# Kernel optimization log

Measured on AMD Instinct MI355X. Metric: run time of the kernel, lower is better.

## Reference

```python
import jax, jax.numpy as jnp
import numpy as np

H = 4  # heads_n (sequential refinement heads)


def _layer_norm(x, g, b, eps=1e-5):
    mu = jnp.mean(x, axis=-1, keepdims=True)
    var = jnp.mean((x - mu) ** 2, axis=-1, keepdims=True)
    return (x - mu) * jax.lax.rsqrt(var + eps) * g + b


def _pose_enc(S, F):
    # Faithful translation of PoseEncoding._make_pe_buffer
    pos = jnp.arange(S, dtype=jnp.float32)[:, None]            # (S,1)
    div = (1.0 / (1000.0 ** (2.0 * jnp.arange(F, dtype=jnp.float32) / F)))[None, :]  # (1,F)
    pe = jnp.zeros((S, F), jnp.float32)
    pe = pe.at[0::2, :].set(jnp.sin(pos[0::2] * div))
    pe = pe.at[1::2, :].set(jnp.cos(pos[1::2] * div))
    return pe  # (S,F)


def setup_inputs() -> dict:
    key = jax.random.key(0)
    ks = jax.random.split(key, 6)
    B, S, C = 4, 2048, 1024
    std = 0.02
    return {
        "x": jax.random.normal(ks[0], (B, S, C), jnp.float32),
        "fc_in_w": jax.random.normal(ks[1], (C, C), jnp.float32) * std,
        "fc_in_b": jnp.zeros((C,), jnp.float32),
        "ln_g": jnp.ones((C,), jnp.float32),
        "ln_b": jnp.zeros((C,), jnp.float32),
        "qkv_w": jax.random.normal(ks[2], (H, 3 * C, C), jnp.float32) * std,
        "qkv_b": jnp.zeros((H, 3 * C), jnp.float32),
        "proj_w": jax.random.normal(ks[3], (H, C, C), jnp.float32) * std,
        "proj_b": jnp.zeros((H, C), jnp.float32),
        "fc_out_w": jax.random.normal(ks[4], (C, C), jnp.float32) * std,
        "fc_out_b": jnp.zeros((C,), jnp.float32),
    }


def reference(x, fc_in_w, fc_in_b, ln_g, ln_b, qkv_w, qkv_b, proj_w, proj_b, fc_out_w, fc_out_b):
    B, S, C = x.shape
    gelu = lambda t: jax.nn.gelu(t, approximate=False)  # nn.GELU default = exact erf
    h = x @ fc_in_w.T + fc_in_b                         # fc_in
    h = _layer_norm(h, ln_g, ln_b)
    pred = None
    for i in range(qkv_w.shape[0]):                     # sequential heads loop (eval mode: dropout = identity)
        qkv = gelu(h @ qkv_w[i].T + qkv_b[i])           # (B,S,3C)
        qkv = qkv.reshape(B, S, 3, C)
        q, k, v = qkv[:, :, 0], qkv[:, :, 1], qkv[:, :, 2]
        scores = jnp.einsum('bsc,btc->bst', q, k) * (1.0 / C)  # (B,S,S), mask is None
        att = jnp.einsum('bst,btc->bsc', scores, v)     # matmul BEFORE softmax (non-standard order)
        att = jax.nn.softmax(att, axis=-1)
        h = gelu(att @ proj_w[i].T + proj_b[i])
        if pred is None:
            pred = h
        else:
            h = h + pred                                 # residual with first head's output
    out = h @ fc_out_w.T + fc_out_b
    return out + _pose_enc(S, out.shape[-1])[None]      # PoseEncoding add
```

## Files before the change

### kernel.cpp

```cpp
#include <hip/hip_runtime.h>
#include <math.h>

typedef unsigned short u16;
typedef __bf16 bf16x8 __attribute__((ext_vector_type(8)));
typedef float f32x4  __attribute__((ext_vector_type(4)));
typedef float f32x16 __attribute__((ext_vector_type(16)));
typedef u16   u16x4  __attribute__((ext_vector_type(4)));
typedef u16   u16x8  __attribute__((ext_vector_type(8)));

#define GPTR(p) ((__attribute__((address_space(1))) void*)(p))
#define LPTR(p) ((__attribute__((address_space(3))) void*)(p))

__device__ __forceinline__ float bf2f(u16 h) { return __uint_as_float(((unsigned)h) << 16); }
__device__ __forceinline__ u16 f2bf(float f) {
    unsigned u = __float_as_uint(f);
    return (u16)((u + 0x7fffu + ((u >> 16) & 1u)) >> 16);
}
__device__ __forceinline__ float gelu_f(float x) {
    float u = 0.7978845608f * x * (1.0f + 0.044715f * x * x);
    float e = __expf(2.0f * u);
    float t = 1.0f - 2.0f / (e + 1.0f);
    return 0.5f * x * (1.0f + t);
}

template<int MODE, int BG>
__global__ __launch_bounds__(256, 4)
void gemm_bt(const u16* __restrict__ A, int lda, long sA,
             const u16* __restrict__ B, int ldb, long sB,
             void* __restrict__ Cout, int ldc, long sC,
             const float* __restrict__ bias,
             const u16* __restrict__ addend,
             int K, float scale)
{
    __shared__ u16 lds[BG ? 8192 : 16384];
    u16* lA = lds;
    u16* lB = lds + 8192;
    const int t    = threadIdx.x;
    const int lane = t & 63;
    const int wid  = t >> 6;
    const int wm   = (wid & 1) * 64;
    const int wn   = (wid >> 1) * 64;
    const int m32  = lane & 31;
    const int h    = lane >> 5;
    const int bz   = blockIdx.z;

    const long rowA0 = (long)blockIdx.y * 128;
    const long colB0 = (long)blockIdx.x * 128;
    const u16* Ab = A + (long)bz * sA + rowA0 * lda;

    const int rt  = t >> 3;
    const int kcg = ((t & 7) ^ (rt & 7)) * 8;
    const u16* gA[4];
    #pragma unroll
    for (int j = 0; j < 4; j++) gA[j] = Ab + (long)(j * 32 + rt) * lda + kcg;
    u16* dA = lA + t * 8;

    const u16* gB[4]; u16* dB = lB + t * 8;
    const u16* gb0 = nullptr; const u16* gb1 = nullptr;
    if constexpr (BG) {
        const int nt0 = (int)((colB0 + wn) >> 5);
        gb0 = B + (long)nt0 * (K >> 4) * 512 + lane * 8;
        gb1 = gb0 + (long)(K >> 4) * 512;
    } else {
        const u16* Bb = B + (long)bz * sB + colB0 * ldb;
        #pragma unroll
        for (int j = 0; j < 4; j++) gB[j] = Bb + (long)(j * 32 + rt) * ldb + kcg;
    }

    f32x16 acc[2][2];
    #pragma unroll
    for (int i = 0; i < 2; i++)
        #pragma unroll
        for (int j = 0; j < 2; j++)
            #pragma unroll
            for (int r = 0; r < 16; r++) acc[i][j][r] = 0.f;

    const int sg = m32 & 7;
    const u16* fA[4]; const u16* fB[4];
    #pragma unroll
    for (int kh = 0; kh < 4; kh++) {
        fA[kh] = lA + (wm + m32) * 64 + 8 * ((kh * 2 + h) ^ sg);
        if constexpr (!BG) fB[kh] = lB + (wn + m32) * 64 + 8 * ((kh * 2 + h) ^ sg);
    }

    for (int k0 = 0; k0 < K; k0 += 64) {
        #pragma unroll
        for (int j = 0; j < 4; j++)
            __builtin_amdgcn_global_load_lds(GPTR(gA[j] + k0), LPTR(dA + j * 2048), 16, 0, 0);
        bf16x8 bg[2][4];
        if constexpr (BG) {
            #pragma unroll
            for (int kh = 0; kh < 4; kh++) {
                bg[0][kh] = *(const bf16x8*)(gb0 + (long)k0 * 32 + kh * 512);
                bg[1][kh] = *(const bf16x8*)(gb1 + (long)k0 * 32 + kh * 512);
            }
        } else {
            #pragma unroll
            for (int j = 0; j < 4; j++)
                __builtin_amdgcn_global_load_lds(GPTR(gB[j] + k0), LPTR(dB + j * 2048), 16, 0, 0);
        }
        __syncthreads();
        #pragma unroll
        for (int kh = 0; kh < 4; kh++) {
            bf16x8 a0 = *(const bf16x8*)(fA[kh]);
            bf16x8 a1 = *(const bf16x8*)(fA[kh] + 2048);
            bf16x8 b0, b1;
            if constexpr (BG) { b0 = bg[0][kh]; b1 = bg[1][kh]; }
            else {
                b0 = *(const bf16x8*)(fB[kh]);
                b1 = *(const bf16x8*)(fB[kh] + 2048);
            }
            acc[0][0] = __builtin_amdgcn_mfma_f32_32x32x16_bf16(a0, b0, acc[0][0], 0, 0, 0);
            acc[0][1] = __builtin_amdgcn_mfma_f32_32x32x16_bf16(a0, b1, acc[0][1], 0, 0, 0);
            acc[1][0] = __builtin_amdgcn_mfma_f32_32x32x16_bf16(a1, b0, acc[1][0], 0, 0, 0);
            acc[1][1] = __builtin_amdgcn_mfma_f32_32x32x16_bf16(a1, b1, acc[1][1], 0, 0, 0);
        }
        __syncthreads();
    }

    float* Cf = (float*)Cout + (long)bz * sC;
    u16*   Cu = (u16*)Cout + (long)bz * sC;
    float* sw_ = (float*)lds + wid * 1024;
    const long rb = rowA0 + wm;
    const long cb = colB0 + wn;
    const int prow = lane >> 3;
    const int c4   = (lane & 7) * 4;
    #pragma unroll
    for (int mi = 0; mi < 2; mi++) {
        #pragma unroll
        for (int ni = 0; ni < 2; ni++) {
            #pragma unroll
            for (int r = 0; r < 16; r++)
                sw_[((r & 3) + 8 * (r >> 2) + 4 * h) * 32 + m32] = acc[mi][ni][r];
            #pragma unroll
            for (int p = 0; p < 4; p++) {
                const int  row  = p * 8 + prow;
                const long grow = rb + mi * 32 + row;
                const long gcol = cb + ni * 32 + c4;
                f32x4 v = *(const f32x4*)&sw_[row * 32 + c4];
                float4 bvv = {0.f, 0.f, 0.f, 0.f};
                if constexpr (MODE >= 2) bvv = *(const float4*)&bias[gcol];
                if constexpr (MODE == 1) {
                    #pragma unroll
                    for (int e = 0; e < 4; e++) v[e] *= scale;
                }
                v[0] += bvv.x; v[1] += bvv.y; v[2] += bvv.z; v[3] += bvv.w;
                if constexpr (MODE == 3 || MODE == 4) {
                    #pragma unroll
                    for (int e = 0; e < 4; e++) v[e] = gelu_f(v[e]);
                }
                if constexpr (MODE == 4) {
                    u16x4 ad = *(const u16x4*)&addend[grow * (long)ldc + gcol];
                    #pragma unroll
                    for (int e = 0; e < 4; e++) v[e] += bf2f(ad[e]);
                }
                if constexpr (MODE == 5) {
                    *(f32x4*)&Cf[grow * (long)ldc + gcol] = v;
                } else {
                    u16x4 o = { f2bf(v[0]), f2bf(v[1]), f2bf(v[2]), f2bf(v[3]) };
                    *(u16x4*)&Cu[grow * (long)ldc + gcol] = o;
                }
            }
        }
    }
}

__global__ __launch_bounds__(256)
void cvt_x(const float* __restrict__ in, u16* __restrict__ out, long n)
{
    long i = ((long)blockIdx.x * 256 + threadIdx.x) * 4;
    if (i < n) {
        float4 v = *(const float4*)(in + i);
        u16x4 o = { f2bf(v.x), f2bf(v.y), f2bf(v.z), f2bf(v.w) };
        *(u16x4*)(out + i) = o;
    }
}

__global__ __launch_bounds__(256)
void cvt_wg(const float* __restrict__ qkvw, u16* __restrict__ dqkv,
            const float* __restrict__ projw, u16* __restrict__ dproj,
            const float* __restrict__ fciw, u16* __restrict__ dfci,
            const float* __restrict__ fcow, u16* __restrict__ dfco)
{
    __shared__ u16 sl[2048];
    const int nt = blockIdx.y;
    const int ks = blockIdx.x;
    const int t  = threadIdx.x;
    const float* src; u16* dst; int nl;
    if      (nt < 384) { src = qkvw;  dst = dqkv;  nl = nt; }
    else if (nt < 512) { src = projw; dst = dproj; nl = nt - 384; }
    else if (nt < 544) { src = fciw;  dst = dfci;  nl = nt - 512; }
    else               { src = fcow;  dst = dfco;  nl = nt - 544; }
    const int n32 = t >> 3;
    const int kq  = t & 7;
    const float* s = src + ((long)nl * 32 + n32) * 1024 + ks * 64 + kq * 8;
    float4 v0 = *(const float4*)s;
    float4 v1 = *(const float4*)(s + 4);
    u16x8 o = { f2bf(v0.x), f2bf(v0.y), f2bf(v0.z), f2bf(v0.w),
                f2bf(v1.x), f2bf(v1.y), f2bf(v1.z), f2bf(v1.w) };
    const int slot = (kq >> 1) * 64 + (kq & 1) * 32 + n32;
    *(u16x8*)&sl[slot * 8] = o;
    __syncthreads();
    u16* d = dst + (long)nl * 32768 + ks * 2048 + t * 8;
    *(u16x8*)d = *(const u16x8*)&sl[t * 8];
}

__global__ __launch_bounds__(256)
void ln_kernel(const u16* __restrict__ in, u16* __restrict__ out,
               const float* __restrict__ g, const float* __restrict__ b)
{
    const int row = blockIdx.x;
    const int t = threadIdx.x;
    const u16* r = in + (long)row * 1024;
    float x[4];
    float s = 0.f, s2 = 0.f;
    #pragma unroll
    for (int j = 0; j < 4; j++) { x[j] = bf2f(r[t + 256 * j]); s += x[j]; s2 += x[j] * x[j]; }
    __shared__ float sm[8];
    const int lane = t & 63, wid = t >> 6;
    #pragma unroll
    for (int o = 32; o > 0; o >>= 1) { s += __shfl_down(s, o, 64); s2 += __shfl_down(s2, o, 64); }
    if (lane == 0) { sm[wid] = s; sm[4 + wid] = s2; }
    __syncthreads();
    s  = sm[0] + sm[1] + sm[2] + sm[3];
    s2 = sm[4] + sm[5] + sm[6] + sm[7];
    const float mean = s * (1.f / 1024.f);
    const float var  = s2 * (1.f / 1024.f) - mean * mean;
    const float rstd = rsqrtf(var + 1e-5f);
    u16* o = out + (long)row * 1024;
    #pragma unroll
    for (int j = 0; j < 4; j++) {
        int c = t + 256 * j;
        o[c] = f2bf((x[j] - mean) * rstd * g[c] + b[c]);
    }
}

__global__ __launch_bounds__(256)
void softmax_kernel(u16* __restrict__ io)
{
    const int row = blockIdx.x;
    const int t = threadIdx.x;
    u16* r = io + (long)row * 1024;
    float x[4];
    float m = -1e30f;
    #pragma unroll
    for (int j = 0; j < 4; j++) { x[j] = bf2f(r[t + 256 * j]); m = fmaxf(m, x[j]); }
    __shared__ float sm[8];
    const int lane = t & 63, wid = t >> 6;
    #pragma unroll
    for (int o = 32; o > 0; o >>= 1) m = fmaxf(m, __shfl_down(m, o, 64));
    if (lane == 0) sm[wid] = m;
    __syncthreads();
    m = fmaxf(fmaxf(sm[0], sm[1]), fmaxf(sm[2], sm[3]));
    float e[4];
    float s = 0.f;
    #pragma unroll
    for (int j = 0; j < 4; j++) { e[j] = __expf(x[j] - m); s += e[j]; }
    #pragma unroll
    for (int o = 32; o > 0; o >>= 1) s += __shfl_down(s, o, 64);
    if (lane == 0) sm[4 + wid] = s;
    __syncthreads();
    s = sm[4] + sm[5] + sm[6] + sm[7];
    const float inv = 1.f / s;
    #pragma unroll
    for (int j = 0; j < 4; j++) r[t + 256 * j] = f2bf(e[j] * inv);
}

__global__ void transpose_v(const u16* __restrict__ qkv, u16* __restrict__ vT)
{
    __shared__ u16 tile[32][33];
    const int b  = blockIdx.z;
    const int t0 = blockIdx.x * 32;
    const int c0 = blockIdx.y * 32;
    const int tx = threadIdx.x, ty = threadIdx.y;
    #pragma unroll
    for (int i = ty; i < 32; i += 8)
        tile[i][tx] = qkv[((long)(b * 2048 + t0 + i)) * 3072 + 2048 + c0 + tx];
    __syncthreads();
    #pragma unroll
    for (int i = ty; i < 32; i += 8)
        vT[((long)(b * 1024 + c0 + i)) * 2048 + t0 + tx] = tile[tx][i];
}

__global__ __launch_bounds__(256)
void add_pe(float* __restrict__ out)
{
    long i = (long)blockIdx.x * 256 + threadIdx.x;
    const int f = (int)(i & 1023);
    const int s = (int)((i >> 10) & 2047);
    const float div = __expf(-(float)f * 0.013491709529261986f);
    const float arg = (float)s * div;
    const float pe = (s & 1) ? cosf(arg) : sinf(arg);
    out[i] += pe;
}

extern "C" void kernel_launch(void* const* d_in, const int* in_sizes, int n_in,
                              void* d_out, int out_size, void* d_ws, size_t ws_size,
                              hipStream_t stream)
{
    const float* x        = (const float*)d_in[0];
    const float* fc_in_w  = (const float*)d_in[1];
    const float* fc_in_b  = (const float*)d_in[2];
    const float* ln_g     = (const float*)d_in[3];
    const float* ln_b     = (const float*)d_in[4];
    const float* qkv_w    = (const float*)d_in[5];
    const float* qkv_b    = (const float*)d_in[6];
    const float* proj_w   = (const float*)d_in[7];
    const float* proj_b   = (const float*)d_in[8];
    const float* fc_out_w = (const float*)d_in[9];
    const float* fc_out_b = (const float*)d_in[10];

    char* w = (char*)d_ws;
    size_t off = 0;
    auto carve = [&](size_t bytes) -> void* {
        void* p = w + off;
        off += (bytes + 255) & ~(size_t)255;
        return p;
    };
    u16* xb   = (u16*)carve(16777216);
    u16* hY   = xb;
    u16* wfci = (u16*)carve(2097152);
    u16* wqkv = (u16*)carve(25165824);
    u16* wprj = (u16*)carve(8388608);
    u16* wfco = (u16*)carve(2097152);
    u16* t0   = (u16*)carve(50331648);
    u16* att  = t0;
    u16* hX   = (u16*)carve(16777216);
    u16* pred = (u16*)carve(16777216);
    u16* vT   = (u16*)carve(16777216);
    u16* sc   = (u16*)carve(33554432);

    cvt_x<<<dim3(8192), dim3(256), 0, stream>>>(x, xb, 8388608L);
    cvt_wg<<<dim3(16, 576), dim3(256), 0, stream>>>(qkv_w, wqkv, proj_w, wprj,
                                                    fc_in_w, wfci, fc_out_w, wfco);

    gemm_bt<2,1><<<dim3(8, 64, 1), 256, 0, stream>>>(xb, 1024, 0, wfci, 0, 0,
                                                     t0, 1024, 0, fc_in_b, nullptr, 1024, 1.0f);
    ln_kernel<<<8192, 256, 0, stream>>>(t0, hX, ln_g, ln_b);

    const u16* hin[4] = { hX, pred, hX, hY };
    u16* hout[4]      = { pred, hX, hY, hX };

    for (int i = 0; i < 4; i++) {
        gemm_bt<3,1><<<dim3(24, 64, 1), 256, 0, stream>>>(hin[i], 1024, 0,
            wqkv + (long)i * 3145728, 0, 0, t0, 3072, 0,
            qkv_b + (long)i * 3072, nullptr, 1024, 1.0f);
        transpose_v<<<dim3(64, 32, 4), dim3(32, 8), 0, stream>>>(t0, vT);
        gemm_bt<1,0><<<dim3(16, 16, 4), 256, 0, stream>>>(t0, 3072, 6291456,
            t0 + 1024, 3072, 6291456, sc, 2048, 4194304,
            nullptr, nullptr, 1024, 1.0f / 1024.0f);
        gemm_bt<0,0><<<dim3(8, 16, 4), 256, 0, stream>>>(sc, 2048, 4194304,
            vT, 2048, 2097152, att, 1024, 2097152,
            nullptr, nullptr, 2048, 1.0f);
        softmax_kernel<<<8192, 256, 0, stream>>>(att);
        if (i == 0)
            gemm_bt<3,1><<<dim3(8, 64, 1), 256, 0, stream>>>(att, 1024, 0,
                wprj, 0, 0, hout[0], 1024, 0, proj_b, nullptr, 1024, 1.0f);
        else
            gemm_bt<4,1><<<dim3(8, 64, 1), 256, 0, stream>>>(att, 1024, 0,
                wprj + (long)i * 1048576, 0, 0, hout[i], 1024, 0,
                proj_b + (long)i * 1024, pred, 1024, 1.0f);
    }

    gemm_bt<5,1><<<dim3(8, 64, 1), 256, 0, stream>>>(hX, 1024, 0, wfco, 0, 0,
                                                     d_out, 1024, 0, fc_out_b, nullptr, 1024, 1.0f);
    add_pe<<<32768, 256, 0, stream>>>((float*)d_out);
}
```

Before: 1.047 ms.

## Write K/V in MFMA fragment layout from QKV epilogue and double-buffer LDS

The QKV GEMM epilogue now writes Q row-major and K and V directly into pre-swizzled MFMA fragment-order buffers. That removes the separate V transpose kernel and lets the score and attention GEMMs stream B operands from global memory into registers instead of staging them in LDS. The GEMM main loop is restructured to double-buffer A tiles in LDS and prefetch the next B fragments, leaving one barrier per iteration. The epilogue applies bias and GELU before an XOR-swizzled LDS staging step. In exchange, occupancy drops (launch bounds 3), register pressure rises, and the score/attention GEMMs now read B straight from global memory rather than from shared LDS tiles.

```diff
diff --git a/kernel.cpp b/kernel.cpp
--- a/kernel.cpp
+++ b/kernel.cpp
@@ -23,18 +23,18 @@
     return 0.5f * x * (1.0f + t);
 }
 
-template<int MODE, int BG>
-__global__ __launch_bounds__(256, 4)
-void gemm_bt(const u16* __restrict__ A, int lda, long sA,
-             const u16* __restrict__ B, int ldb, long sB,
-             void* __restrict__ Cout, int ldc, long sC,
-             const float* __restrict__ bias,
-             const u16* __restrict__ addend,
-             int K, float scale)
-{
-    __shared__ u16 lds[BG ? 8192 : 16384];
+template<int MODE>
+__global__ __launch_bounds__(256, 3)
+void gemm_g(const u16* __restrict__ A, int lda, long sA,
+            const u16* __restrict__ B, long sB,
+            void* __restrict__ Cout, int ldc, long sC,
+            const float* __restrict__ bias,
+            const u16* __restrict__ addend,
+            u16* __restrict__ kgr, u16* __restrict__ vgr,
+            int K, float scale)
+{
+    __shared__ u16 lds[16384];
     u16* lA = lds;
-    u16* lB = lds + 8192;
     const int t    = threadIdx.x;
     const int lane = t & 63;
     const int wid  = t >> 6;
@@ -55,17 +55,10 @@
     for (int j = 0; j < 4; j++) gA[j] = Ab + (long)(j * 32 + rt) * lda + kcg;
     u16* dA = lA + t * 8;
 
-    const u16* gB[4]; u16* dB = lB + t * 8;
-    const u16* gb0 = nullptr; const u16* gb1 = nullptr;
-    if constexpr (BG) {
-        const int nt0 = (int)((colB0 + wn) >> 5);
-        gb0 = B + (long)nt0 * (K >> 4) * 512 + lane * 8;
-        gb1 = gb0 + (long)(K >> 4) * 512;
-    } else {
-        const u16* Bb = B + (long)bz * sB + colB0 * ldb;
-        #pragma unroll
-        for (int j = 0; j < 4; j++) gB[j] = Bb + (long)(j * 32 + rt) * ldb + kcg;
-    }
+    const int nt0 = (int)((colB0 + wn) >> 5);
+    const long ktn = (long)(K >> 4) * 512;
+    const u16* gb0 = B + (long)bz * sB + (long)nt0 * ktn + lane * 8;
+    const u16* gb1 = gb0 + ktn;
 
     f32x16 acc[2][2];
     #pragma unroll
@@ -76,46 +69,49 @@
             for (int r = 0; r < 16; r++) acc[i][j][r] = 0.f;
 
     const int sg = m32 & 7;
-    const u16* fA[4]; const u16* fB[4];
+    const u16* fA[4];
+    #pragma unroll
+    for (int kh = 0; kh < 4; kh++)
+        fA[kh] = lA + (wm + m32) * 64 + 8 * ((kh * 2 + h) ^ sg);
+
+    #pragma unroll
+    for (int j = 0; j < 4; j++)
+        __builtin_amdgcn_global_load_lds(GPTR(gA[j]), LPTR(dA + j * 2048), 16, 0, 0);
+    bf16x8 bc[2][4], bn[2][4];
     #pragma unroll
     for (int kh = 0; kh < 4; kh++) {
-        fA[kh] = lA + (wm + m32) * 64 + 8 * ((kh * 2 + h) ^ sg);
-        if constexpr (!BG) fB[kh] = lB + (wn + m32) * 64 + 8 * ((kh * 2 + h) ^ sg);
-    }
-
-    for (int k0 = 0; k0 < K; k0 += 64) {
-        #pragma unroll
-        for (int j = 0; j < 4; j++)
-            __builtin_amdgcn_global_load_lds(GPTR(gA[j] + k0), LPTR(dA + j * 2048), 16, 0, 0);
-        bf16x8 bg[2][4];
-        if constexpr (BG) {
+        bc[0][kh] = *(const bf16x8*)(gb0 + kh * 512);
+        bc[1][kh] = *(const bf16x8*)(gb1 + kh * 512);
+    }
+
+    const int niter = K >> 6;
+    for (int it = 0; it < niter; ++it) {
+        __syncthreads();
+        const int kn = (it + 1) << 6;
+        if (kn < K) {
+            const int nb = (it + 1) & 1;
+            #pragma unroll
+            for (int j = 0; j < 4; j++)
+                __builtin_amdgcn_global_load_lds(GPTR(gA[j] + kn),
+                                                 LPTR(dA + nb * 8192 + j * 2048), 16, 0, 0);
             #pragma unroll
             for (int kh = 0; kh < 4; kh++) {
-                bg[0][kh] = *(const bf16x8*)(gb0 + (long)k0 * 32 + kh * 512);
-                bg[1][kh] = *(const bf16x8*)(gb1 + (long)k0 * 32 + kh * 512);
+                bn[0][kh] = *(const bf16x8*)(gb0 + (long)kn * 32 + kh * 512);
+                bn[1][kh] = *(const bf16x8*)(gb1 + (long)kn * 32 + kh * 512);
             }
-        } else {
-            #pragma unroll
-            for (int j = 0; j < 4; j++)
-                __builtin_amdgcn_global_load_lds(GPTR(gB[j] + k0), LPTR(dB + j * 2048), 16, 0, 0);
         }
-        __syncthreads();
+        const int cbo = (it & 1) * 8192;
         #pragma unroll
         for (int kh = 0; kh < 4; kh++) {
-            bf16x8 a0 = *(const bf16x8*)(fA[kh]);
-            bf16x8 a1 = *(const bf16x8*)(fA[kh] + 2048);
-            bf16x8 b0, b1;
-            if constexpr (BG) { b0 = bg[0][kh]; b1 = bg[1][kh]; }
-            else {
-                b0 = *(const bf16x8*)(fB[kh]);
-                b1 = *(const bf16x8*)(fB[kh] + 2048);
-            }
-            acc[0][0] = __builtin_amdgcn_mfma_f32_32x32x16_bf16(a0, b0, acc[0][0], 0, 0, 0);
-            acc[0][1] = __builtin_amdgcn_mfma_f32_32x32x16_bf16(a0, b1, acc[0][1], 0, 0, 0);
-            acc[1][0] = __builtin_amdgcn_mfma_f32_32x32x16_bf16(a1, b0, acc[1][0], 0, 0, 0);
-            acc[1][1] = __builtin_amdgcn_mfma_f32_32x32x16_bf16(a1, b1, acc[1][1], 0, 0, 0);
+            bf16x8 a0 = *(const bf16x8*)(fA[kh] + cbo);
+            bf16x8 a1 = *(const bf16x8*)(fA[kh] + cbo + 2048);
+            acc[0][0] = __builtin_amdgcn_mfma_f32_32x32x16_bf16(a0, bc[0][kh], acc[0][0], 0, 0, 0);
+            acc[0][1] = __builtin_amdgcn_mfma_f32_32x32x16_bf16(a0, bc[1][kh], acc[0][1], 0, 0, 0);
+            acc[1][0] = __builtin_amdgcn_mfma_f32_32x32x16_bf16(a1, bc[0][kh], acc[1][0], 0, 0, 0);
+            acc[1][1] = __builtin_amdgcn_mfma_f32_32x32x16_bf16(a1, bc[1][kh], acc[1][1], 0, 0, 0);
         }
-        __syncthreads();
+        #pragma unroll
+        for (int kh = 0; kh < 4; kh++) { bc[0][kh] = bn[0][kh]; bc[1][kh] = bn[1][kh]; }
     }
 
     float* Cf = (float*)Cout + (long)bz * sC;
@@ -129,36 +125,70 @@
     for (int mi = 0; mi < 2; mi++) {
         #pragma unroll
         for (int ni = 0; ni < 2; ni++) {
+            const int colg = (int)(cb + ni * 32 + m32);
+            float bv = 0.0f;
+            if constexpr (MODE >= 2) bv = bias[colg];
             #pragma unroll
-            for (int r = 0; r < 16; r++)
-                sw_[((r & 3) + 8 * (r >> 2) + 4 * h) * 32 + m32] = acc[mi][ni][r];
-            #pragma unroll
-            for (int p = 0; p < 4; p++) {
-                const int  row  = p * 8 + prow;
-                const long grow = rb + mi * 32 + row;
-                const long gcol = cb + ni * 32 + c4;
-                f32x4 v = *(const f32x4*)&sw_[row * 32 + c4];
-                float4 bvv = {0.f, 0.f, 0.f, 0.f};
-                if constexpr (MODE >= 2) bvv = *(const float4*)&bias[gcol];
-                if constexpr (MODE == 1) {
+            for (int r = 0; r < 16; r++) {
+                float v = acc[mi][ni][r];
+                if constexpr (MODE == 1) v *= scale;
+                v += bv;
+                if constexpr (MODE == 3 || MODE == 4 || MODE == 6) v = gelu_f(v);
+                const int rowfn = (r & 3) + 8 * (r >> 2) + 4 * h;
+                sw_[rowfn * 32 + (m32 ^ ((rowfn & 3) * 8))] = v;
+            }
+            const int seg = (MODE == 6) ? (int)(colB0 >> 10) : 0;
+            if (MODE != 6 || seg == 0) {
+                #pragma unroll
+                for (int p = 0; p < 4; p++) {
+                    const int  row  = p * 8 + prow;
+                    const long grow = rb + mi * 32 + row;
+                    const long gcol = cb + ni * 32 + c4;
+                    const int  key  = (row & 3) * 8;
+                    f32x4 v = *(const f32x4*)&sw_[row * 32 + (c4 ^ key)];
+                    if constexpr (MODE == 4) {
+                        u16x4 ad = *(const u16x4*)&addend[grow * (long)ldc + gcol];
+                        #pragma unroll
+                        for (int e = 0; e < 4; e++) v[e] += bf2f(ad[e]);
+                    }
+                    if constexpr (MODE == 5) {
+                        *(f32x4*)&Cf[grow * (long)ldc + gcol] = v;
+                    } else {
+                        u16x4 o = { f2bf(v[0]), f2bf(v[1]), f2bf(v[2]), f2bf(v[3]) };
+                        *(u16x4*)&Cu[grow * (long)ldc + gcol] = o;
+                    }
+                }
+            } else if (seg == 1) {
+                const int b   = (int)(rb >> 11);
+                const int nt  = ((int)(rb & 2047) + mi * 32) >> 5;
+                const int kt0 = ((int)cb + ni * 32 - 1024) >> 4;
+                u16* base = kgr + (long)b * 2097152 + ((long)(nt * 64 + kt0) * 64 + lane) * 8;
+                #pragma unroll
+                for (int q2 = 0; q2 < 2; q2++) {
+                    const int g0  = q2 * 16 + h * 8;
+                    const int key = (m32 & 3) * 8;
+                    f32x4 u0 = *(const f32x4*)&sw_[m32 * 32 + (g0 ^ key)];
+                    f32x4 u1 = *(const f32x4*)&sw_[m32 * 32 + (g0 ^ key) + 4];
+                    u16x8 o = { f2bf(u0[0]), f2bf(u0[1]), f2bf(u0[2]), f2bf(u0[3]),
+                                f2bf(u1[0]), f2bf(u1[1]), f2bf(u1[2]), f2bf(u1[3]) };
+                    *(u16x8*)(base + q2 * 512) = o;
+                }
+            } else {
+                const int b   = (int)(rb >> 11);
+                const int kt0 = ((int)(rb & 2047) + mi * 32) >> 4;
+                const int nt  = ((int)cb + ni * 32 - 2048) >> 5;
+                u16* base = vgr + (long)b * 2097152 + ((long)(nt * 128 + kt0) * 64 + lane) * 8;
+                #pragma unroll
+                for (int q2 = 0; q2 < 2; q2++) {
+                    float vv[8];
                     #pragma unroll
-                    for (int e = 0; e < 4; e++) v[e] *= scale;
-                }
-                v[0] += bvv.x; v[1] += bvv.y; v[2] += bvv.z; v[3] += bvv.w;
-                if constexpr (MODE == 3 || MODE == 4) {
-                    #pragma unroll
-                    for (int e = 0; e < 4; e++) v[e] = gelu_f(v[e]);
-                }
-                if constexpr (MODE == 4) {
-                    u16x4 ad = *(const u16x4*)&addend[grow * (long)ldc + gcol];
-                    #pragma unroll
-                    for (int e = 0; e < 4; e++) v[e] += bf2f(ad[e]);
-                }
-                if constexpr (MODE == 5) {
-                    *(f32x4*)&Cf[grow * (long)ldc + gcol] = v;
-                } else {
-                    u16x4 o = { f2bf(v[0]), f2bf(v[1]), f2bf(v[2]), f2bf(v[3]) };
-                    *(u16x4*)&Cu[grow * (long)ldc + gcol] = o;
+                    for (int j = 0; j < 8; j++) {
+                        const int r = q2 * 16 + h * 8 + j;
+                        vv[j] = sw_[r * 32 + (m32 ^ ((r & 3) * 8))];
+                    }
+                    u16x8 o = { f2bf(vv[0]), f2bf(vv[1]), f2bf(vv[2]), f2bf(vv[3]),
+                                f2bf(vv[4]), f2bf(vv[5]), f2bf(vv[6]), f2bf(vv[7]) };
+                    *(u16x8*)(base + q2 * 512) = o;
                 }
             }
         }
@@ -266,22 +296,6 @@
     for (int j = 0; j < 4; j++) r[t + 256 * j] = f2bf(e[j] * inv);
 }
 
-__global__ void transpose_v(const u16* __restrict__ qkv, u16* __restrict__ vT)
-{
-    __shared__ u16 tile[32][33];
-    const int b  = blockIdx.z;
-    const int t0 = blockIdx.x * 32;
-    const int c0 = blockIdx.y * 32;
-    const int tx = threadIdx.x, ty = threadIdx.y;
-    #pragma unroll
-    for (int i = ty; i < 32; i += 8)
-        tile[i][tx] = qkv[((long)(b * 2048 + t0 + i)) * 3072 + 2048 + c0 + tx];
-    __syncthreads();
-    #pragma unroll
-    for (int i = ty; i < 32; i += 8)
-        vT[((long)(b * 1024 + c0 + i)) * 2048 + t0 + tx] = tile[tx][i];
-}
-
 __global__ __launch_bounds__(256)
 void add_pe(float* __restrict__ out)
 {
@@ -323,46 +337,46 @@
     u16* wqkv = (u16*)carve(25165824);
     u16* wprj = (u16*)carve(8388608);
     u16* wfco = (u16*)carve(2097152);
-    u16* t0   = (u16*)carve(50331648);
-    u16* att  = t0;
+    u16* qb   = (u16*)carve(16777216);
+    u16* kgr  = (u16*)carve(16777216);
+    u16* vgr  = (u16*)carve(16777216);
+    u16* att  = (u16*)carve(16777216);
     u16* hX   = (u16*)carve(16777216);
     u16* pred = (u16*)carve(16777216);
-    u16* vT   = (u16*)carve(16777216);
     u16* sc   = (u16*)carve(33554432);
 
     cvt_x<<<dim3(8192), dim3(256), 0, stream>>>(x, xb, 8388608L);
     cvt_wg<<<dim3(16, 576), dim3(256), 0, stream>>>(qkv_w, wqkv, proj_w, wprj,
                                                     fc_in_w, wfci, fc_out_w, wfco);
 
-    gemm_bt<2,1><<<dim3(8, 64, 1), 256, 0, stream>>>(xb, 1024, 0, wfci, 0, 0,
-                                                     t0, 1024, 0, fc_in_b, nullptr, 1024, 1.0f);
-    ln_kernel<<<8192, 256, 0, stream>>>(t0, hX, ln_g, ln_b);
+    gemm_g<2><<<dim3(8, 64, 1), 256, 0, stream>>>(xb, 1024, 0, wfci, 0,
+        qb, 1024, 0, fc_in_b, nullptr, nullptr, nullptr, 1024, 1.0f);
+    ln_kernel<<<8192, 256, 0, stream>>>(qb, hX, ln_g, ln_b);
 
     const u16* hin[4] = { hX, pred, hX, hY };
     u16* hout[4]      = { pred, hX, hY, hX };
 
     for (int i = 0; i < 4; i++) {
-        gemm_bt<3,1><<<dim3(24, 64, 1), 256, 0, stream>>>(hin[i], 1024, 0,
-            wqkv + (long)i * 3145728, 0, 0, t0, 3072, 0,
-            qkv_b + (long)i * 3072, nullptr, 1024, 1.0f);
-        transpose_v<<<dim3(64, 32, 4), dim3(32, 8), 0, stream>>>(t0, vT);
-        gemm_bt<1,0><<<dim3(16, 16, 4), 256, 0, stream>>>(t0, 3072, 6291456,
-            t0 + 1024, 3072, 6291456, sc, 2048, 4194304,
-            nullptr, nullptr, 1024, 1.0f / 1024.0f);
-        gemm_bt<0,0><<<dim3(8, 16, 4), 256, 0, stream>>>(sc, 2048, 4194304,
-            vT, 2048, 2097152, att, 1024, 2097152,
-            nullptr, nullptr, 2048, 1.0f);
+        gemm_g<6><<<dim3(24, 64, 1), 256, 0, stream>>>(hin[i], 1024, 0,
+            wqkv + (long)i * 3145728, 0, qb, 1024, 0,
+            qkv_b + (long)i * 3072, nullptr, kgr, vgr, 1024, 1.0f);
+        gemm_g<1><<<dim3(16, 16, 4), 256, 0, stream>>>(qb, 1024, 2097152,
+            kgr, 2097152, sc, 2048, 4194304,
+            nullptr, nullptr, nullptr, nullptr, 1024, 1.0f / 1024.0f);
+        gemm_g<0><<<dim3(8, 16, 4), 256, 0, stream>>>(sc, 2048, 4194304,
+            vgr, 2097152, att, 1024, 2097152,
+            nullptr, nullptr, nullptr, nullptr, 2048, 1.0f);
         softmax_kernel<<<8192, 256, 0, stream>>>(att);
         if (i == 0)
-            gemm_bt<3,1><<<dim3(8, 64, 1), 256, 0, stream>>>(att, 1024, 0,
-                wprj, 0, 0, hout[0], 1024, 0, proj_b, nullptr, 1024, 1.0f);
+            gemm_g<3><<<dim3(8, 64, 1), 256, 0, stream>>>(att, 1024, 0,
+                wprj, 0, hout[0], 1024, 0, proj_b, nullptr, nullptr, nullptr, 1024, 1.0f);
         else
-            gemm_bt<4,1><<<dim3(8, 64, 1), 256, 0, stream>>>(att, 1024, 0,
-                wprj + (long)i * 1048576, 0, 0, hout[i], 1024, 0,
-                proj_b + (long)i * 1024, pred, 1024, 1.0f);
-    }
-
-    gemm_bt<5,1><<<dim3(8, 64, 1), 256, 0, stream>>>(hX, 1024, 0, wfco, 0, 0,
-                                                     d_out, 1024, 0, fc_out_b, nullptr, 1024, 1.0f);
+            gemm_g<4><<<dim3(8, 64, 1), 256, 0, stream>>>(att, 1024, 0,
+                wprj + (long)i * 1048576, 0, hout[i], 1024, 0,
+                proj_b + (long)i * 1024, pred, nullptr, nullptr, 1024, 1.0f);
+    }
+
+    gemm_g<5><<<dim3(8, 64, 1), 256, 0, stream>>>(hX, 1024, 0, wfco, 0,
+        d_out, 1024, 0, fc_out_b, nullptr, nullptr, nullptr, 1024, 1.0f);
     add_pe<<<32768, 256, 0, stream>>>((float*)d_out);
 }
```

After: 1.045 ms. No clear change (-0.1%).
